# Kernel optimization log

Measured on AMD Instinct MI355X. Metric: run time of the kernel, lower is better.

## Reference

```python
import jax, jax.numpy as jnp
import numpy as np

D_MODEL = 512
N_HEADS = 8
HEAD_DIM = D_MODEL // N_HEADS
SEQ = 2048
BATCH = 2
EPS = 1e-5
SCALE = 1.0 / np.sqrt(HEAD_DIM).astype(np.float32)
# (kind, window, dilation) per head, matching init_kwargs head_specs
SPECS = [("global", 0, 1), ("global", 0, 1),
         ("window", 64, 1), ("window", 128, 1), ("window", 256, 1),
         ("dilated", 64, 2), ("dilated", 64, 4), ("dilated", 64, 8)]


def build_masks(N):
    i = jnp.arange(N)
    D = jnp.abs(i[:, None] - i[None, :])
    ms = []
    for kind, w, dil in SPECS:
        if kind == "global":
            ms.append(jnp.ones((N, N), dtype=bool))
        elif kind == "window":
            ms.append(D <= w)
        else:  # dilated
            ms.append((D % dil == 0) & (D // dil <= w))
    return jnp.stack(ms)  # [H, N, N] bool


def layernorm(x, g, b):
    mu = jnp.mean(x, axis=-1, keepdims=True)
    var = jnp.mean((x - mu) ** 2, axis=-1, keepdims=True)
    return (x - mu) * jax.lax.rsqrt(var + EPS) * g + b


def setup_inputs() -> dict:
    key = jax.random.key(0)
    ks = jax.random.split(key, 7)
    w = 0.02
    return {
        "x": jax.random.normal(ks[0], (BATCH, SEQ, D_MODEL), dtype=jnp.float32),
        "Wq": jax.random.normal(ks[1], (D_MODEL, D_MODEL), dtype=jnp.float32) * w,
        "Wk": jax.random.normal(ks[2], (D_MODEL, D_MODEL), dtype=jnp.float32) * w,
        "Wv": jax.random.normal(ks[3], (D_MODEL, D_MODEL), dtype=jnp.float32) * w,
        "Wo": jax.random.normal(ks[4], (D_MODEL, D_MODEL), dtype=jnp.float32) * w,
        "T_w1": jax.random.normal(ks[5], (D_MODEL, D_MODEL), dtype=jnp.float32) * w,
        "T_b1": jnp.zeros((D_MODEL,), dtype=jnp.float32),
        "T_w2": jax.random.normal(ks[6], (1, D_MODEL), dtype=jnp.float32) * w,
        "T_b2": jnp.zeros((1,), dtype=jnp.float32),
        "ln_in_g": jnp.ones((D_MODEL,), dtype=jnp.float32),
        "ln_in_b": jnp.zeros((D_MODEL,), dtype=jnp.float32),
        "ln_out_g": jnp.ones((D_MODEL,), dtype=jnp.float32),
        "ln_out_b": jnp.zeros((D_MODEL,), dtype=jnp.float32),
    }


def reference(x, Wq, Wk, Wv, Wo, T_w1, T_b1, T_w2, T_b2,
              ln_in_g, ln_in_b, ln_out_g, ln_out_b):
    B, N, H = x.shape
    x0 = x
    xn = layernorm(x, ln_in_g, ln_in_b)
    # torch Linear: y = x @ W.T ; reshape to [B, h, N, d]
    def heads(W):
        return (xn @ W.T).reshape(B, N, N_HEADS, HEAD_DIM).transpose(0, 2, 1, 3)
    Q, K, V = heads(Wq), heads(Wk), heads(Wv)
    attn = jnp.einsum("bhqd,bhkd->bhqk", Q, K) * SCALE
    mask = build_masks(N)  # [h, N, N]
    attn = jnp.where(mask[None], attn, -jnp.inf)
    attn = jax.nn.softmax(attn, axis=-1)  # every row has diagonal unmasked
    out = jnp.einsum("bhqk,bhkd->bhqd", attn, V)
    out = out.transpose(0, 2, 1, 3).reshape(B, N, N_HEADS * HEAD_DIM)
    out = out @ Wo.T
    # tanh-gated softmax over sequence dim
    T_logits = jnp.tanh(xn @ T_w1.T + T_b1) @ T_w2.T + T_b2  # [B, N, 1]
    T = jax.nn.softmax(T_logits, axis=1)
    out = out * T
    return layernorm(out + x0, ln_out_g, ln_out_b)
```

## Files before the change

kernel.cpp:

```cpp
#include <hip/hip_runtime.h>
#include <math.h>

#define N_SEQ 2048
#define DM    512
#define NTOK  4096
#define NH    8
#define HD    64
#define NSLOT 18

typedef __attribute__((ext_vector_type(8))) short short8;
typedef __attribute__((ext_vector_type(4))) short short4_t;
typedef __attribute__((ext_vector_type(4))) float f32x4;

__device__ inline short f2bf(float x) {
    union { float f; unsigned u; } v; v.f = x;
    unsigned r = v.u + 0x7fff + ((v.u >> 16) & 1);
    return (short)(r >> 16);
}
__device__ inline float bf2f(short s) {
    union { unsigned u; float f; } v; v.u = ((unsigned)(unsigned short)s) << 16;
    return v.f;
}
__device__ inline unsigned pkbf(float a, float b) {
    return ((unsigned)(unsigned short)f2bf(b) << 16) | (unsigned)(unsigned short)f2bf(a);
}
__device__ inline float ftanh(float x) {
    float e = __expf(2.f * x);
    return 1.f - 2.f / (e + 1.f);
}

__device__ inline f32x4 mfma16(short8 a, short8 b, f32x4 c) {
    return __builtin_amdgcn_mfma_f32_16x16x32_bf16(a, b, c, 0, 0, 0);
}

__device__ __forceinline__ void async_cp16(const short* g, short* l) {
    __builtin_amdgcn_global_load_lds(
        (const __attribute__((address_space(1))) void*)g,
        (__attribute__((address_space(3))) void*)l, 16, 0, 0);
}

__global__ __launch_bounds__(256) void k_lncvt(
    const float* __restrict__ x, const float* __restrict__ g,
    const float* __restrict__ b, short* __restrict__ y, float* __restrict__ lg,
    const float* __restrict__ Wq, const float* __restrict__ Wk,
    const float* __restrict__ Wv, const float* __restrict__ Tw1,
    const float* __restrict__ Wo,
    short* __restrict__ wcat, short* __restrict__ wo) {
    int blk = blockIdx.x, t = threadIdx.x;
    if (blk < 2048) {
        int sub = t >> 7, tt = t & 127;
        int tk = blk * 2 + sub;
        if (tt == 0) lg[tk] = 0.f;
        float4 xv = ((const float4*)(x + (size_t)tk * DM))[tt];
        float s = xv.x + xv.y + xv.z + xv.w;
        float q = xv.x*xv.x + xv.y*xv.y + xv.z*xv.z + xv.w*xv.w;
        for (int o = 32; o; o >>= 1) { s += __shfl_down(s, o); q += __shfl_down(q, o); }
        __shared__ float ls[4], lq[4];
        if ((t & 63) == 0) { ls[t >> 6] = s; lq[t >> 6] = q; }
        __syncthreads();
        s = ls[sub * 2] + ls[sub * 2 + 1];
        q = lq[sub * 2] + lq[sub * 2 + 1];
        float mu = s * (1.f / DM);
        float var = q * (1.f / DM) - mu * mu;
        float rs = rsqrtf(var + 1e-5f);
        float4 gv = ((const float4*)g)[tt], bv = ((const float4*)b)[tt];
        short4_t o;
        o[0] = f2bf((xv.x - mu) * rs * gv.x + bv.x);
        o[1] = f2bf((xv.y - mu) * rs * gv.y + bv.y);
        o[2] = f2bf((xv.z - mu) * rs * gv.z + bv.z);
        o[3] = f2bf((xv.w - mu) * rs * gv.w + bv.w);
        *(short4_t*)&y[(size_t)tk * DM + tt * 4] = o;
    } else {
        int id = (blk - 2048) * 256 + t;
        if (id < 262144) {
            int z = id >> 16; int off = id & 65535;
            const float* s = (z == 0) ? Wq : (z == 1) ? Wk : (z == 2) ? Wv : Tw1;
            float4 v = ((const float4*)s)[off];
            short4_t o = {f2bf(v.x), f2bf(v.y), f2bf(v.z), f2bf(v.w)};
            *(short4_t*)(wcat + (size_t)z * 262144 + (size_t)off * 4) = o;
        } else {
            int off = id - 262144;
            float4 v = ((const float4*)Wo)[off];
            short4_t o = {f2bf(v.x), f2bf(v.y), f2bf(v.z), f2bf(v.w)};
            *(short4_t*)(wo + (size_t)off * 4) = o;
        }
    }
}

__global__ __launch_bounds__(256) void k_gemmqkvt(
    const short* __restrict__ A, const short* __restrict__ W,
    const float* __restrict__ Tb1, const float* __restrict__ Tw2,
    short* __restrict__ qb, short* __restrict__ kb, short* __restrict__ vtb,
    float* __restrict__ lg) {
    __shared__ short As[128 * 32];
    __shared__ short Bs[128 * 32];
    __shared__ short Vs[128 * 136];
    int t = threadIdx.x;
    int lane = t & 63, w = t >> 6;
    int wy = w >> 1, wx = w & 1;
    int ln = lane & 15, q4 = lane >> 4;
    int c0 = blockIdx.x * 128, m0 = blockIdx.y * 128;
    int sr = t >> 2, sc = (t & 3) << 3;
    f32x4 acc[4][4];
    f32x4 zero = {0.f, 0.f, 0.f, 0.f};
    #pragma unroll
    for (int i = 0; i < 4; i++)
        #pragma unroll
        for (int j = 0; j < 4; j++) acc[i][j] = zero;
    for (int k0 = 0; k0 < DM; k0 += 32) {
        __syncthreads();
        async_cp16(&A[(size_t)(m0 + sr) * DM + k0 + sc],      &As[sr * 32 + sc]);
        async_cp16(&A[(size_t)(m0 + 64 + sr) * DM + k0 + sc], &As[(64 + sr) * 32 + sc]);
        async_cp16(&W[(size_t)(c0 + sr) * DM + k0 + sc],      &Bs[sr * 32 + sc]);
        async_cp16(&W[(size_t)(c0 + 64 + sr) * DM + k0 + sc], &Bs[(64 + sr) * 32 + sc]);
        __syncthreads();
        short8 af[4], bfr[4];
        #pragma unroll
        for (int i = 0; i < 4; i++)
            af[i] = *(short8*)&As[(wy * 64 + i * 16 + ln) * 32 + q4 * 8];
        #pragma unroll
        for (int j = 0; j < 4; j++)
            bfr[j] = *(short8*)&Bs[(wx * 64 + j * 16 + ln) * 32 + q4 * 8];
        #pragma unroll
        for (int i = 0; i < 4; i++)
            #pragma unroll
            for (int j = 0; j < 4; j++)
                acc[i][j] = mfma16(af[i], bfr[j], acc[i][j]);
    }
    int z = c0 >> 9;
    if (z < 2) {
        short* dst = (z == 0) ? qb : kb;
        float sc2 = (z == 0) ? 0.125f : 1.0f;
        #pragma unroll
        for (int i = 0; i < 4; i++)
            #pragma unroll
            for (int j = 0; j < 4; j++)
                #pragma unroll
                for (int r = 0; r < 4; r++) {
                    int row = m0 + wy * 64 + i * 16 + q4 * 4 + r;
                    int col = c0 + wx * 64 + j * 16 + ln;
                    int nin = col & 511;
                    int h = nin >> 6, d = nin & 63;
                    int bi = row >> 11, n = row & (N_SEQ - 1);
                    dst[(((size_t)bi * NH + h) * N_SEQ + n) * HD + d] =
                        f2bf(acc[i][j][r] * sc2);
                }
    } else if (z == 2) {
        #pragma unroll
        for (int i = 0; i < 4; i++)
            #pragma unroll
            for (int j = 0; j < 4; j++)
                #pragma unroll
                for (int r = 0; r < 4; r++) {
                    int nl = wy * 64 + i * 16 + q4 * 4 + r;
                    int dl = wx * 64 + j * 16 + ln;
                    Vs[dl * 136 + nl] = f2bf(acc[i][j][r]);
                }
        __syncthreads();
        int bi = m0 >> 11, n0 = m0 & (N_SEQ - 1);
        int hp = (c0 & 511) >> 6;
        #pragma unroll
        for (int ii = 0; ii < 8; ii++) {
            int id = t + 256 * ii;
            int dl = id >> 4, nc = id & 15;
            short8 v = *(short8*)&Vs[dl * 136 + nc * 8];
            int h = hp + (dl >> 6), d = dl & 63;
            *(short8*)&vtb[(((size_t)bi * NH + h) * HD + d) * N_SEQ + n0 + nc * 8] = v;
        }
    } else {
        #pragma unroll
        for (int i = 0; i < 4; i++) {
            #pragma unroll
            for (int r = 0; r < 4; r++) {
                float s = 0.f;
                #pragma unroll
                for (int j = 0; j < 4; j++) {
                    int tc = (c0 & 511) + wx * 64 + j * 16 + ln;
                    s += ftanh(acc[i][j][r] + Tb1[tc]) * Tw2[tc];
                }
                s += __shfl_xor(s, 1);
                s += __shfl_xor(s, 2);
                s += __shfl_xor(s, 4);
                s += __shfl_xor(s, 8);
                if (ln == 0) {
                    int row = m0 + wy * 64 + i * 16 + q4 * 4 + r;
                    atomicAdd(&lg[row], s);
                }
            }
        }
    }
}

__global__ __launch_bounds__(256) void k_gemmp(
    const short* __restrict__ A, const short* __restrict__ W,
    float* __restrict__ proj) {
    __shared__ short As[128 * 32];
    __shared__ short Bs[64 * 32];
    int t = threadIdx.x;
    int lane = t & 63, w = t >> 6;
    int wy = w >> 1, wx = w & 1;
    int ln = lane & 15, q4 = lane >> 4;
    int c0 = blockIdx.x * 64, m0 = blockIdx.y * 128;
    int sr = t >> 2, sc = (t & 3) << 3;
    int br = t >> 2, bc = (t & 3) << 3;
    f32x4 acc[4][2];
    f32x4 zero = {0.f, 0.f, 0.f, 0.f};
    #pragma unroll
    for (int i = 0; i < 4; i++) { acc[i][0] = zero; acc[i][1] = zero; }
    for (int k0 = 0; k0 < DM; k0 += 32) {
        __syncthreads();
        async_cp16(&A[(size_t)(m0 + sr) * DM + k0 + sc],      &As[sr * 32 + sc]);
        async_cp16(&A[(size_t)(m0 + 64 + sr) * DM + k0 + sc], &As[(64 + sr) * 32 + sc]);
        if (br < 64)
            async_cp16(&W[(size_t)(c0 + br) * DM + k0 + bc], &Bs[br * 32 + bc]);
        __syncthreads();
        short8 af[4], bfr[2];
        #pragma unroll
        for (int i = 0; i < 4; i++)
            af[i] = *(short8*)&As[(wy * 64 + i * 16 + ln) * 32 + q4 * 8];
        #pragma unroll
        for (int j = 0; j < 2; j++)
            bfr[j] = *(short8*)&Bs[(wx * 32 + j * 16 + ln) * 32 + q4 * 8];
        #pragma unroll
        for (int i = 0; i < 4; i++)
            #pragma unroll
            for (int j = 0; j < 2; j++)
                acc[i][j] = mfma16(af[i], bfr[j], acc[i][j]);
    }
    #pragma unroll
    for (int i = 0; i < 4; i++)
        #pragma unroll
        for (int j = 0; j < 2; j++)
            #pragma unroll
            for (int r = 0; r < 4; r++) {
                int row = m0 + wy * 64 + i * 16 + q4 * 4 + r;
                int col = c0 + wx * 32 + j * 16 + ln;
                proj[(size_t)row * DM + col] = acc[i][j][r];
            }
}

__global__ __launch_bounds__(256) void k_attn(const short* __restrict__ qb,
                                              const short* __restrict__ kb,
                                              const short* __restrict__ vtb,
                                              short* __restrict__ P_O,
                                              float* __restrict__ P_ml,
                                              short* __restrict__ ob,
                                              const float* __restrict__ lg,
                                              float* __restrict__ gate) {
    __shared__ short Ks[128 * 72];
    __shared__ short Vt[64 * 136];
    __shared__ short Pa[4][16 * 136];
    __shared__ float rg[8];
    int t = threadIdx.x;
    int lane = t & 63, w = t >> 6;
    int ln = lane & 15, q4 = lane >> 4;
    int slot = blockIdx.x, qt = blockIdx.y, bi = blockIdx.z;
    int q0 = qt * 64;
    int h, c;
    if (slot < 4)        { h = 0; c = slot; }
    else if (slot < 8)   { h = 1; c = slot - 4; }
    else if (slot == 8)  { h = 2; c = 0; }
    else if (slot == 9)  { h = 3; c = 0; }
    else if (slot < 12)  { h = 4; c = slot - 10; }
    else if (slot == 12) { h = 5; c = 0; }
    else if (slot < 15)  { h = 6; c = slot - 13; }
    else                 { h = 7; c = slot - 15; }
    int solo = (slot == 8) | (slot == 9) | (slot == 12);
    int kind = (h < 2) ? 0 : (h < 5) ? 1 : 2;
    int wnd = (h == 2 || h >= 5) ? 64 : (h == 3) ? 128 : (h == 4) ? 256 : 0;
    int dsh = (h == 5) ? 1 : (h == 6) ? 2 : (h == 7) ? 3 : 0;
    int dmask = (1 << dsh) - 1;
    int wmax = (kind == 0) ? 0 : (wnd << dsh);
    int tLoU, tHiU, CS;
    if (kind == 0) { tLoU = 0; tHiU = 15; CS = 4; }
    else { tLoU = (q0 - wmax) >> 7; tHiU = (q0 + 63 + wmax) >> 7; CS = 3; }
    int ktLo = tLoU + c * CS;
    int ktHi = ktLo + CS - 1;
    if (ktHi > tHiU) ktHi = tHiU;
    if (ktHi > 15) ktHi = 15;
    if (ktLo < 0) ktLo = 0;
    int p4 = (bi * 32 + qt) * NSLOT + slot;
    float* ml = P_ml + (size_t)p4 * 128;
    if (ktLo > ktHi) {
        if (t < 64) { ml[t] = -1e30f; ml[64 + t] = 0.f; }
        return;
    }
    const size_t base = ((size_t)bi * NH + h) * N_SEQ * HD;
    const short* Q = qb + base;
    const short* K = kb + base;
    const short* Vg = vtb + base;
    short8 qa[2];
    {
        const short* qrow = Q + (size_t)(q0 + w * 16 + ln) * HD + q4 * 8;
        qa[0] = *(const short8*)qrow;
        qa[1] = *(const short8*)(qrow + 32);
    }
    int qi = q0 + w * 16 + ln;
    float m_i = -1e30f, l_i = 0.f;
    f32x4 OT[4];
    f32x4 zero = {0.f, 0.f, 0.f, 0.f};
    #pragma unroll
    for (int d = 0; d < 4; d++) OT[d] = zero;
    short* Paw = Pa[w];
    for (int kt = ktLo; kt <= ktHi; kt++) {
        int k0 = kt << 7;
        __syncthreads();
        #pragma unroll
        for (int i2 = 0; i2 < 4; i2++) {
            int id = t + 256 * i2;
            int kr = id >> 3, cc = id & 7;
            *(short8*)&Ks[kr * 72 + cc * 8] =
                *(const short8*)&K[(size_t)(k0 + kr) * HD + cc * 8];
            int dr = id >> 4, kc = id & 15;
            *(short8*)&Vt[dr * 136 + kc * 8] =
                *(const short8*)&Vg[(size_t)dr * N_SEQ + k0 + kc * 8];
        }
        __syncthreads();
        f32x4 ST[8];
        #pragma unroll
        for (int nt = 0; nt < 8; nt++) ST[nt] = zero;
        #pragma unroll
        for (int nt = 0; nt < 8; nt++) {
            #pragma unroll
            for (int ks = 0; ks < 2; ks++) {
                short8 af = *(short8*)&Ks[(nt * 16 + ln) * 72 + ks * 32 + q4 * 8];
                ST[nt] = mfma16(af, qa[ks], ST[nt]);
            }
        }
        if (kind != 0) {
            #pragma unroll
            for (int nt = 0; nt < 8; nt++)
                #pragma unroll
                for (int r = 0; r < 4; r++) {
                    int key = k0 + nt * 16 + q4 * 4 + r;
                    int dlt = qi - key; dlt = (dlt < 0) ? -dlt : dlt;
                    int valid;
                    if (kind == 1) valid = (dlt <= wnd);
                    else valid = ((dlt & dmask) == 0) && ((dlt >> dsh) <= wnd);
                    if (!valid) ST[nt][r] = -1e30f;
                }
        }
        float rm = -1e30f;
        #pragma unroll
        for (int nt = 0; nt < 8; nt++) {
            float a = fmaxf(ST[nt][0], ST[nt][1]);
            float b = fmaxf(ST[nt][2], ST[nt][3]);
            rm = fmaxf(rm, fmaxf(a, b));
        }
        rm = fmaxf(rm, __shfl_xor(rm, 16));
        rm = fmaxf(rm, __shfl_xor(rm, 32));
        float mn = fmaxf(m_i, rm);
        float sc = __expf(m_i - mn);
        float rs = 0.f;
        #pragma unroll
        for (int nt = 0; nt < 8; nt++) {
            float p0 = __expf(ST[nt][0] - mn);
            float p1 = __expf(ST[nt][1] - mn);
            float p2 = __expf(ST[nt][2] - mn);
            float p3 = __expf(ST[nt][3] - mn);
            rs += (p0 + p1) + (p2 + p3);
            *(unsigned*)&Paw[ln * 136 + nt * 16 + q4 * 4]     = pkbf(p0, p1);
            *(unsigned*)&Paw[ln * 136 + nt * 16 + q4 * 4 + 2] = pkbf(p2, p3);
        }
        rs += __shfl_xor(rs, 16);
        rs += __shfl_xor(rs, 32);
        l_i = l_i * sc + rs;
        m_i = mn;
        #pragma unroll
        for (int d = 0; d < 4; d++) OT[d] *= sc;
        short8 pb[4];
        #pragma unroll
        for (int ks = 0; ks < 4; ks++)
            pb[ks] = *(short8*)&Paw[ln * 136 + ks * 32 + q4 * 8];
        #pragma unroll
        for (int dt = 0; dt < 4; dt++) {
            #pragma unroll
            for (int ks = 0; ks < 4; ks++) {
                short8 a = *(short8*)&Vt[(dt * 16 + ln) * 136 + ks * 32 + q4 * 8];
                OT[dt] = mfma16(a, pb[ks], OT[dt]);
            }
        }
    }
    if (solo) {
        float inv = 1.f / l_i;
        #pragma unroll
        for (int dt = 0; dt < 4; dt++) {
            *(unsigned*)&Paw[ln * 136 + dt * 16 + q4 * 4]     = pkbf(OT[dt][0] * inv, OT[dt][1] * inv);
            *(unsigned*)&Paw[ln * 136 + dt * 16 + q4 * 4 + 2] = pkbf(OT[dt][2] * inv, OT[dt][3] * inv);
        }
        short8 o0 = *(short8*)&Paw[ln * 136 + q4 * 16];
        short8 o1 = *(short8*)&Paw[ln * 136 + q4 * 16 + 8];
        short* dst = ob + ((size_t)bi * N_SEQ + q0 + w * 16 + ln) * DM + h * 64 + q4 * 16;
        *(short8*)dst = o0;
        *(short8*)(dst + 8) = o1;
    } else {
        if (q4 == 0) { ml[w * 16 + ln] = m_i; ml[64 + w * 16 + ln] = l_i; }
        #pragma unroll
        for (int dt = 0; dt < 4; dt++) {
            *(unsigned*)&Paw[ln * 136 + dt * 16 + q4 * 4]     = pkbf(OT[dt][0], OT[dt][1]);
            *(unsigned*)&Paw[ln * 136 + dt * 16 + q4 * 4 + 2] = pkbf(OT[dt][2], OT[dt][3]);
        }
        short8 o0 = *(short8*)&Paw[ln * 136 + q4 * 16];
        short8 o1 = *(short8*)&Paw[ln * 136 + q4 * 16 + 8];
        short* Op = P_O + (size_t)p4 * 4096;
        *(short8*)&Op[(w * 16 + ln) * 64 + q4 * 16] = o0;
        *(short8*)&Op[(w * 16 + ln) * 64 + q4 * 16 + 8] = o1;
    }
    if (slot == 8 && qt == 0) {
        int b = bi;
        float v[8];
        float4 a0 = *(const float4*)&lg[b * N_SEQ + t * 8];
        float4 a1 = *(const float4*)&lg[b * N_SEQ + t * 8 + 4];
        v[0] = a0.x; v[1] = a0.y; v[2] = a0.z; v[3] = a0.w;
        v[4] = a1.x; v[5] = a1.y; v[6] = a1.z; v[7] = a1.w;
        float m = v[0];
        #pragma unroll
        for (int j = 1; j < 8; j++) m = fmaxf(m, v[j]);
        for (int o = 32; o; o >>= 1) m = fmaxf(m, __shfl_down(m, o));
        if ((t & 63) == 0) rg[t >> 6] = m;
        __syncthreads();
        m = fmaxf(fmaxf(rg[0], rg[1]), fmaxf(rg[2], rg[3]));
        float e[8], s = 0.f;
        #pragma unroll
        for (int j = 0; j < 8; j++) { e[j] = __expf(v[j] - m); s += e[j]; }
        for (int o = 32; o; o >>= 1) s += __shfl_down(s, o);
        if ((t & 63) == 0) rg[4 + (t >> 6)] = s;
        __syncthreads();
        s = (rg[4] + rg[5]) + (rg[6] + rg[7]);
        float inv = 1.f / s;
        float4 o0 = {e[0] * inv, e[1] * inv, e[2] * inv, e[3] * inv};
        float4 o1 = {e[4] * inv, e[5] * inv, e[6] * inv, e[7] * inv};
        *(float4*)&gate[b * N_SEQ + t * 8] = o0;
        *(float4*)&gate[b * N_SEQ + t * 8 + 4] = o1;
    }
}

__global__ __launch_bounds__(256) void k_combine(const short* __restrict__ P_O,
                                                 const float* __restrict__ P_ml,
                                                 short* __restrict__ ob) {
    const int hsel[5]  = {0, 1, 4, 6, 7};
    const int hbase[5] = {0, 4, 10, 13, 15};
    const int hcnt[5]  = {4, 4, 2, 2, 3};
    int hh = blockIdx.x, qt = blockIdx.y, bi = blockIdx.z;
    int h = hsel[hh];
    int t = threadIdx.x;
    int row = t >> 2, c0 = (t & 3) * 16;
    int pb = (bi * 32 + qt) * NSLOT + hbase[hh];
    int cnt = hcnt[hh];
    float m = -1e30f;
    for (int s = 0; s < cnt; s++)
        m = fmaxf(m, P_ml[(size_t)(pb + s) * 128 + row]);
    float l = 0.f;
    float acc[16];
    #pragma unroll
    for (int j = 0; j < 16; j++) acc[j] = 0.f;
    for (int s = 0; s < cnt; s++) {
        float ms = P_ml[(size_t)(pb + s) * 128 + row];
        float ls = P_ml[(size_t)(pb + s) * 128 + 64 + row];
        if (ls > 0.f) {
            float sc = __expf(ms - m);
            l += ls * sc;
            const short* Op = P_O + (size_t)(pb + s) * 4096 + row * 64 + c0;
            short8 v0 = *(const short8*)Op;
            short8 v1 = *(const short8*)(Op + 8);
            #pragma unroll
            for (int j = 0; j < 8; j++) acc[j]     += bf2f(v0[j]) * sc;
            #pragma unroll
            for (int j = 0; j < 8; j++) acc[8 + j] += bf2f(v1[j]) * sc;
        }
    }
    float inv = 1.f / l;
    int n = qt * 64 + row;
    short8 o0, o1;
    #pragma unroll
    for (int j = 0; j < 8; j++) o0[j] = f2bf(acc[j] * inv);
    #pragma unroll
    for (int j = 0; j < 8; j++) o1[j] = f2bf(acc[8 + j] * inv);
    short* dst = ob + ((size_t)bi * N_SEQ + n) * DM + h * 64 + c0;
    *(short8*)dst = o0;
    *(short8*)(dst + 8) = o1;
}

__global__ __launch_bounds__(128) void k_final(const float* __restrict__ proj,
                                               const float* __restrict__ gate,
                                               const float* __restrict__ x0,
                                               const float* __restrict__ g,
                                               const float* __restrict__ b,
                                               float* __restrict__ out) {
    int tk = blockIdx.x, t = threadIdx.x;
    float gt = gate[tk];
    float4 pv = ((const float4*)(proj + (size_t)tk * DM))[t];
    float4 xv = ((const float4*)(x0 + (size_t)tk * DM))[t];
    float4 y;
    y.x = pv.x * gt + xv.x;
    y.y = pv.y * gt + xv.y;
    y.z = pv.z * gt + xv.z;
    y.w = pv.w * gt + xv.w;
    float s = y.x + y.y + y.z + y.w;
    float q = y.x*y.x + y.y*y.y + y.z*y.z + y.w*y.w;
    for (int o = 32; o; o >>= 1) { s += __shfl_down(s, o); q += __shfl_down(q, o); }
    __shared__ float ls[2], lq[2];
    if ((t & 63) == 0) { ls[t >> 6] = s; lq[t >> 6] = q; }
    __syncthreads();
    s = ls[0] + ls[1]; q = lq[0] + lq[1];
    float mu = s * (1.f / DM);
    float var = q * (1.f / DM) - mu * mu;
    float rs = rsqrtf(var + 1e-5f);
    float4 gv = ((const float4*)g)[t], bv = ((const float4*)b)[t];
    float4 o;
    o.x = (y.x - mu) * rs * gv.x + bv.x;
    o.y = (y.y - mu) * rs * gv.y + bv.y;
    o.z = (y.z - mu) * rs * gv.z + bv.z;
    o.w = (y.w - mu) * rs * gv.w + bv.w;
    ((float4*)(out + (size_t)tk * DM))[t] = o;
}

extern "C" void kernel_launch(void* const* d_in, const int* in_sizes, int n_in,
                              void* d_out, int out_size, void* d_ws, size_t ws_size,
                              hipStream_t stream) {
    (void)in_sizes; (void)n_in; (void)out_size; (void)ws_size;
    const float* x    = (const float*)d_in[0];
    const float* Wq   = (const float*)d_in[1];
    const float* Wk   = (const float*)d_in[2];
    const float* Wv   = (const float*)d_in[3];
    const float* Wo   = (const float*)d_in[4];
    const float* Tw1  = (const float*)d_in[5];
    const float* Tb1  = (const float*)d_in[6];
    const float* Tw2  = (const float*)d_in[7];
    const float* ling = (const float*)d_in[9];
    const float* linb = (const float*)d_in[10];
    const float* logg = (const float*)d_in[11];
    const float* logb = (const float*)d_in[12];
    float* out = (float*)d_out;

    const size_t SZ = (size_t)NTOK * DM;
    const int NPART = 2 * 32 * NSLOT;
    char* p = (char*)d_ws;
    short* xn   = (short*)p; p += SZ * 2;
    short* wcat = (short*)p; p += (size_t)2048 * DM * 2;
    short* wo   = (short*)p; p += (size_t)DM * DM * 2;
    short* qb   = (short*)p; p += SZ * 2;
    short* kb   = (short*)p; p += SZ * 2;
    short* vtb  = (short*)p; p += SZ * 2;
    short* obuf = (short*)p; p += SZ * 2;
    float* lg   = (float*)p; p += (size_t)NTOK * 4;
    float* gate = (float*)p; p += (size_t)NTOK * 4;
    float* P_ml = (float*)p; p += (size_t)NPART * 128 * 4;
    float* proj = (float*)p;
    short* P_O  = (short*)p; p += (size_t)NPART * 4096 * 2;

    k_lncvt<<<3328, 256, 0, stream>>>(x, ling, linb, xn, lg,
                                      Wq, Wk, Wv, Tw1, Wo, wcat, wo);
    k_gemmqkvt<<<dim3(16, 32), 256, 0, stream>>>(xn, wcat, Tb1, Tw2,
                                                 qb, kb, vtb, lg);
    k_attn<<<dim3(NSLOT, 32, 2), 256, 0, stream>>>(qb, kb, vtb, P_O, P_ml,
                                                   obuf, lg, gate);
    k_combine<<<dim3(5, 32, 2), 256, 0, stream>>>(P_O, P_ml, obuf);
    k_gemmp<<<dim3(8, 32), 256, 0, stream>>>(obuf, wo, proj);
    k_final<<<NTOK, 128, 0, stream>>>(proj, gate, x, logg, logb, out);
}
```

Baseline: 159.0 us.

## Double-buffer GEMM tiles, stage Q/K epilogue via LDS, swizzle attention K/V loads

Both projection GEMMs now double-buffer their LDS tiles, prefetching the next K-slice with async copies while the MFMAs run on the current one, with one barrier per iteration instead of two. The Q/K epilogue is staged through shared memory so global stores become 16-byte vectors, and the V-transpose writes use packed pairs. The attention kernel loads K and V tiles with async copies into XOR-swizzled, unpadded LDS layouts, and raises wave priority around the MFMA blocks. This adds LDS footprint and index arithmetic, and a swizzle mistake would corrupt results.

```diff
diff --git a/kernel.cpp b/kernel.cpp
--- a/kernel.cpp
+++ b/kernel.cpp
@@ -92,9 +92,7 @@
     const float* __restrict__ Tb1, const float* __restrict__ Tw2,
     short* __restrict__ qb, short* __restrict__ kb, short* __restrict__ vtb,
     float* __restrict__ lg) {
-    __shared__ short As[128 * 32];
-    __shared__ short Bs[128 * 32];
-    __shared__ short Vs[128 * 136];
+    __shared__ short smem[17408];
     int t = threadIdx.x;
     int lane = t & 63, w = t >> 6;
     int wy = w >> 1, wx = w & 1;
@@ -107,45 +105,47 @@
     for (int i = 0; i < 4; i++)
         #pragma unroll
         for (int j = 0; j < 4; j++) acc[i][j] = zero;
-    for (int k0 = 0; k0 < DM; k0 += 32) {
-        __syncthreads();
-        async_cp16(&A[(size_t)(m0 + sr) * DM + k0 + sc],      &As[sr * 32 + sc]);
-        async_cp16(&A[(size_t)(m0 + 64 + sr) * DM + k0 + sc], &As[(64 + sr) * 32 + sc]);
-        async_cp16(&W[(size_t)(c0 + sr) * DM + k0 + sc],      &Bs[sr * 32 + sc]);
-        async_cp16(&W[(size_t)(c0 + 64 + sr) * DM + k0 + sc], &Bs[(64 + sr) * 32 + sc]);
-        __syncthreads();
+    {
+        short* AsB = smem; short* BsB = smem + 4096;
+        async_cp16(&A[(size_t)(m0 + sr) * DM + sc],      &AsB[sr * 32 + sc]);
+        async_cp16(&A[(size_t)(m0 + 64 + sr) * DM + sc], &AsB[(64 + sr) * 32 + sc]);
+        async_cp16(&W[(size_t)(c0 + sr) * DM + sc],      &BsB[sr * 32 + sc]);
+        async_cp16(&W[(size_t)(c0 + 64 + sr) * DM + sc], &BsB[(64 + sr) * 32 + sc]);
+    }
+    __syncthreads();
+    for (int kk = 0; kk < 16; kk++) {
+        short* AsB = &smem[(kk & 1) * 8192];
+        short* BsB = AsB + 4096;
+        if (kk < 15) {
+            short* AsN = &smem[((kk & 1) ^ 1) * 8192];
+            short* BsN = AsN + 4096;
+            int k0 = (kk + 1) * 32;
+            async_cp16(&A[(size_t)(m0 + sr) * DM + k0 + sc],      &AsN[sr * 32 + sc]);
+            async_cp16(&A[(size_t)(m0 + 64 + sr) * DM + k0 + sc], &AsN[(64 + sr) * 32 + sc]);
+            async_cp16(&W[(size_t)(c0 + sr) * DM + k0 + sc],      &BsN[sr * 32 + sc]);
+            async_cp16(&W[(size_t)(c0 + 64 + sr) * DM + k0 + sc], &BsN[(64 + sr) * 32 + sc]);
+        }
         short8 af[4], bfr[4];
         #pragma unroll
         for (int i = 0; i < 4; i++)
-            af[i] = *(short8*)&As[(wy * 64 + i * 16 + ln) * 32 + q4 * 8];
+            af[i] = *(short8*)&AsB[(wy * 64 + i * 16 + ln) * 32 + q4 * 8];
         #pragma unroll
         for (int j = 0; j < 4; j++)
-            bfr[j] = *(short8*)&Bs[(wx * 64 + j * 16 + ln) * 32 + q4 * 8];
+            bfr[j] = *(short8*)&BsB[(wx * 64 + j * 16 + ln) * 32 + q4 * 8];
         #pragma unroll
         for (int i = 0; i < 4; i++)
             #pragma unroll
             for (int j = 0; j < 4; j++)
                 acc[i][j] = mfma16(af[i], bfr[j], acc[i][j]);
-    }
+        __syncthreads();
+    }
+    short* Es = smem;
     int z = c0 >> 9;
+    int bi = m0 >> 11, n0 = m0 & (N_SEQ - 1);
+    int hp = (c0 & 511) >> 6;
     if (z < 2) {
-        short* dst = (z == 0) ? qb : kb;
+        short* dst0 = (z == 0) ? qb : kb;
         float sc2 = (z == 0) ? 0.125f : 1.0f;
-        #pragma unroll
-        for (int i = 0; i < 4; i++)
-            #pragma unroll
-            for (int j = 0; j < 4; j++)
-                #pragma unroll
-                for (int r = 0; r < 4; r++) {
-                    int row = m0 + wy * 64 + i * 16 + q4 * 4 + r;
-                    int col = c0 + wx * 64 + j * 16 + ln;
-                    int nin = col & 511;
-                    int h = nin >> 6, d = nin & 63;
-                    int bi = row >> 11, n = row & (N_SEQ - 1);
-                    dst[(((size_t)bi * NH + h) * N_SEQ + n) * HD + d] =
-                        f2bf(acc[i][j][r] * sc2);
-                }
-    } else if (z == 2) {
         #pragma unroll
         for (int i = 0; i < 4; i++)
             #pragma unroll
@@ -153,17 +153,34 @@
                 #pragma unroll
                 for (int r = 0; r < 4; r++) {
                     int nl = wy * 64 + i * 16 + q4 * 4 + r;
-                    int dl = wx * 64 + j * 16 + ln;
-                    Vs[dl * 136 + nl] = f2bf(acc[i][j][r]);
+                    int cl = wx * 64 + j * 16 + ln;
+                    Es[nl * 136 + cl] = f2bf(acc[i][j][r] * sc2);
                 }
         __syncthreads();
-        int bi = m0 >> 11, n0 = m0 & (N_SEQ - 1);
-        int hp = (c0 & 511) >> 6;
+        #pragma unroll
+        for (int ii = 0; ii < 8; ii++) {
+            int id = t + 256 * ii;
+            int nl = id >> 4, c8 = id & 15;
+            short8 v = *(short8*)&Es[nl * 136 + c8 * 8];
+            int hh = hp + (c8 >> 3), d8 = (c8 & 7) * 8;
+            *(short8*)&dst0[(((size_t)bi * NH + hh) * N_SEQ + n0 + nl) * HD + d8] = v;
+        }
+    } else if (z == 2) {
+        #pragma unroll
+        for (int i = 0; i < 4; i++)
+            #pragma unroll
+            for (int j = 0; j < 4; j++) {
+                int nl0 = wy * 64 + i * 16 + q4 * 4;
+                int dl = wx * 64 + j * 16 + ln;
+                *(unsigned*)&Es[dl * 136 + nl0]     = pkbf(acc[i][j][0], acc[i][j][1]);
+                *(unsigned*)&Es[dl * 136 + nl0 + 2] = pkbf(acc[i][j][2], acc[i][j][3]);
+            }
+        __syncthreads();
         #pragma unroll
         for (int ii = 0; ii < 8; ii++) {
             int id = t + 256 * ii;
             int dl = id >> 4, nc = id & 15;
-            short8 v = *(short8*)&Vs[dl * 136 + nc * 8];
+            short8 v = *(short8*)&Es[dl * 136 + nc * 8];
             int h = hp + (dl >> 6), d = dl & 63;
             *(short8*)&vtb[(((size_t)bi * NH + h) * HD + d) * N_SEQ + n0 + nc * 8] = v;
         }
@@ -194,38 +211,48 @@
 __global__ __launch_bounds__(256) void k_gemmp(
     const short* __restrict__ A, const short* __restrict__ W,
     float* __restrict__ proj) {
-    __shared__ short As[128 * 32];
-    __shared__ short Bs[64 * 32];
+    __shared__ short smem[12288];
     int t = threadIdx.x;
     int lane = t & 63, w = t >> 6;
     int wy = w >> 1, wx = w & 1;
     int ln = lane & 15, q4 = lane >> 4;
     int c0 = blockIdx.x * 64, m0 = blockIdx.y * 128;
     int sr = t >> 2, sc = (t & 3) << 3;
-    int br = t >> 2, bc = (t & 3) << 3;
     f32x4 acc[4][2];
     f32x4 zero = {0.f, 0.f, 0.f, 0.f};
     #pragma unroll
     for (int i = 0; i < 4; i++) { acc[i][0] = zero; acc[i][1] = zero; }
-    for (int k0 = 0; k0 < DM; k0 += 32) {
-        __syncthreads();
-        async_cp16(&A[(size_t)(m0 + sr) * DM + k0 + sc],      &As[sr * 32 + sc]);
-        async_cp16(&A[(size_t)(m0 + 64 + sr) * DM + k0 + sc], &As[(64 + sr) * 32 + sc]);
-        if (br < 64)
-            async_cp16(&W[(size_t)(c0 + br) * DM + k0 + bc], &Bs[br * 32 + bc]);
-        __syncthreads();
+    {
+        short* AsB = smem; short* BsB = smem + 4096;
+        async_cp16(&A[(size_t)(m0 + sr) * DM + sc],      &AsB[sr * 32 + sc]);
+        async_cp16(&A[(size_t)(m0 + 64 + sr) * DM + sc], &AsB[(64 + sr) * 32 + sc]);
+        async_cp16(&W[(size_t)(c0 + sr) * DM + sc],      &BsB[sr * 32 + sc]);
+    }
+    __syncthreads();
+    for (int kk = 0; kk < 16; kk++) {
+        short* AsB = &smem[(kk & 1) * 6144];
+        short* BsB = AsB + 4096;
+        if (kk < 15) {
+            short* AsN = &smem[((kk & 1) ^ 1) * 6144];
+            short* BsN = AsN + 4096;
+            int k0 = (kk + 1) * 32;
+            async_cp16(&A[(size_t)(m0 + sr) * DM + k0 + sc],      &AsN[sr * 32 + sc]);
+            async_cp16(&A[(size_t)(m0 + 64 + sr) * DM + k0 + sc], &AsN[(64 + sr) * 32 + sc]);
+            async_cp16(&W[(size_t)(c0 + sr) * DM + k0 + sc],      &BsN[sr * 32 + sc]);
+        }
         short8 af[4], bfr[2];
         #pragma unroll
         for (int i = 0; i < 4; i++)
-            af[i] = *(short8*)&As[(wy * 64 + i * 16 + ln) * 32 + q4 * 8];
+            af[i] = *(short8*)&AsB[(wy * 64 + i * 16 + ln) * 32 + q4 * 8];
         #pragma unroll
         for (int j = 0; j < 2; j++)
-            bfr[j] = *(short8*)&Bs[(wx * 32 + j * 16 + ln) * 32 + q4 * 8];
+            bfr[j] = *(short8*)&BsB[(wx * 32 + j * 16 + ln) * 32 + q4 * 8];
         #pragma unroll
         for (int i = 0; i < 4; i++)
             #pragma unroll
             for (int j = 0; j < 2; j++)
                 acc[i][j] = mfma16(af[i], bfr[j], acc[i][j]);
+        __syncthreads();
     }
     #pragma unroll
     for (int i = 0; i < 4; i++)
@@ -247,8 +274,8 @@
                                               short* __restrict__ ob,
                                               const float* __restrict__ lg,
                                               float* __restrict__ gate) {
-    __shared__ short Ks[128 * 72];
-    __shared__ short Vt[64 * 136];
+    __shared__ short Ks[128 * 64];
+    __shared__ short Vt[64 * 128];
     __shared__ short Pa[4][16 * 136];
     __shared__ float rg[8];
     int t = threadIdx.x;
@@ -308,25 +335,28 @@
         #pragma unroll
         for (int i2 = 0; i2 < 4; i2++) {
             int id = t + 256 * i2;
-            int kr = id >> 3, cc = id & 7;
-            *(short8*)&Ks[kr * 72 + cc * 8] =
-                *(const short8*)&K[(size_t)(k0 + kr) * HD + cc * 8];
-            int dr = id >> 4, kc = id & 15;
-            *(short8*)&Vt[dr * 136 + kc * 8] =
-                *(const short8*)&Vg[(size_t)dr * N_SEQ + k0 + kc * 8];
+            int kr = id >> 3, ck = id & 7;
+            async_cp16(&K[(size_t)(k0 + kr) * HD + ((ck ^ (kr & 7)) << 3)],
+                       &Ks[id << 3]);
+            int dr = id >> 4, cv = id & 15;
+            async_cp16(&Vg[(size_t)dr * N_SEQ + k0 + ((cv ^ (dr & 15)) << 3)],
+                       &Vt[id << 3]);
         }
         __syncthreads();
         f32x4 ST[8];
         #pragma unroll
         for (int nt = 0; nt < 8; nt++) ST[nt] = zero;
+        __builtin_amdgcn_s_setprio(1);
         #pragma unroll
         for (int nt = 0; nt < 8; nt++) {
             #pragma unroll
             for (int ks = 0; ks < 2; ks++) {
-                short8 af = *(short8*)&Ks[(nt * 16 + ln) * 72 + ks * 32 + q4 * 8];
+                int cc = ((ks * 4 + q4) ^ (ln & 7)) << 3;
+                short8 af = *(short8*)&Ks[(nt * 16 + ln) * 64 + cc];
                 ST[nt] = mfma16(af, qa[ks], ST[nt]);
             }
         }
+        __builtin_amdgcn_s_setprio(0);
         if (kind != 0) {
             #pragma unroll
             for (int nt = 0; nt < 8; nt++)
@@ -372,14 +402,17 @@
         #pragma unroll
         for (int ks = 0; ks < 4; ks++)
             pb[ks] = *(short8*)&Paw[ln * 136 + ks * 32 + q4 * 8];
+        __builtin_amdgcn_s_setprio(1);
         #pragma unroll
         for (int dt = 0; dt < 4; dt++) {
             #pragma unroll
             for (int ks = 0; ks < 4; ks++) {
-                short8 a = *(short8*)&Vt[(dt * 16 + ln) * 136 + ks * 32 + q4 * 8];
+                int cc = ((ks * 4 + q4) ^ ln) << 3;
+                short8 a = *(short8*)&Vt[(dt * 16 + ln) * 128 + cc];
                 OT[dt] = mfma16(a, pb[ks], OT[dt]);
             }
         }
+        __builtin_amdgcn_s_setprio(0);
     }
     if (solo) {
         float inv = 1.f / l_i;
```

New measurement: 154.5 us (median of 2 runs). 2.8% less time.
